# Performance work log

Measured on AMD Instinct MI355X. Metric: run time of the kernel, lower is better.

The kernel has to match this reference:

```python
import jax, jax.numpy as jnp
from jax import lax
import numpy as np
import math

_DN = ('NCHW', 'OIHW', 'NCHW')
_SIGMA = 1.0
_RADIUS = int(4.0 * _SIGMA + 0.5)  # scipy truncate=4.0 default


def _gauss_kernel():
    x = jnp.arange(-_RADIUS, _RADIUS + 1, dtype=jnp.float32)
    k = jnp.exp(-0.5 * x * x / (_SIGMA * _SIGMA))
    return k / k.sum()


def _gaussian_filter(m):
    # m: [B,C,H,W]; scipy mode='reflect' == numpy pad mode 'symmetric'
    B, C, H, W = m.shape
    k = _gauss_kernel()
    x = m.reshape(B * C, 1, H, W)
    xp = jnp.pad(x, ((0, 0), (0, 0), (_RADIUS, _RADIUS), (0, 0)), mode='symmetric')
    x = lax.conv_general_dilated(xp, k.reshape(1, 1, 2 * _RADIUS + 1, 1), (1, 1), 'VALID', dimension_numbers=_DN)
    xp = jnp.pad(x, ((0, 0), (0, 0), (0, 0), (_RADIUS, _RADIUS)), mode='symmetric')
    x = lax.conv_general_dilated(xp, k.reshape(1, 1, 1, 2 * _RADIUS + 1), (1, 1), 'VALID', dimension_numbers=_DN)
    return x.reshape(B, C, H, W)


def _sobel_mag_dir(x):
    C = x.shape[1]
    sx = jnp.array([[-1, 0, 1], [-2, 0, 2], [-1, 0, 1]], dtype=jnp.float32).reshape(1, 1, 3, 3)
    sy = jnp.array([[-1, -2, -1], [0, 0, 0], [1, 2, 1]], dtype=jnp.float32).reshape(1, 1, 3, 3)
    kx = jnp.tile(sx, (C, 1, 1, 1))
    ky = jnp.tile(sy, (C, 1, 1, 1))
    gx = lax.conv_general_dilated(x, kx, (1, 1), ((1, 1), (1, 1)), dimension_numbers=_DN, feature_group_count=C)
    gy = lax.conv_general_dilated(x, ky, (1, 1), ((1, 1), (1, 1)), dimension_numbers=_DN, feature_group_count=C)
    mag = jnp.sqrt(gx * gx + gy * gy + 1e-8)
    direction = jnp.arctan2(gy, gx)
    return mag, direction


def _boundary_weight(mask_f):
    sm = jnp.clip(_gaussian_filter(mask_f), 0.0, 1.0)
    bw = 1.0 - jnp.abs(sm - 0.5) / 0.5
    return jnp.clip(bw, 0.0, 1.0)


def setup_inputs() -> dict:
    key = jax.random.key(0)
    k1, k2, k3 = jax.random.split(key, 3)
    B, C, H, W = 8, 3, 512, 512
    output = jax.random.normal(k1, (B, C, H, W), dtype=jnp.float32)
    target = jax.random.normal(k2, (B, C, H, W), dtype=jnp.float32)
    mask = jax.random.randint(k3, (B, C, H, W), 0, 2, dtype=jnp.int32)
    return {"output": output, "target": target, "mask": mask}


def reference(output, target, mask):
    mask_f = mask.astype(jnp.float32)
    out_mag, out_dir = _sobel_mag_dir(output)
    tgt_mag, tgt_dir = _sobel_mag_dir(target)
    w = _boundary_weight(mask_f)

    mag_loss = jnp.mean(jnp.abs(out_mag * w - tgt_mag * w))
    wsum = w.sum()
    mag_loss = jnp.where(wsum > 0, mag_loss / (w.mean() + 1e-8), mag_loss)

    dd = jnp.abs(out_dir - tgt_dir)
    dd = jnp.minimum(dd, 2 * math.pi - dd)
    dir_loss = (dd * w).sum()
    dir_loss = jnp.where(wsum > 0, dir_loss / (wsum + 1e-8), dir_loss)

    return mag_loss + dir_loss
```

## Files before the change

### kernel.cpp

```cpp
#include <hip/hip_runtime.h>
#include <math.h>

#define HH 512
#define WW 512
#define NBC 24
#define TH 64
#define TW 32
#define RAD 4
#define NXT (WW / TW)
#define NYT (HH / TH)
#define NBLK (NXT * NYT * NBC)
#define PI_F 3.14159265358979323846f
#define SMW 36
#define OTW 40

__device__ __constant__ float GW[9] = {
    1.3383023e-04f, 4.4318484e-03f, 5.3990968e-02f, 2.4197073e-01f,
    3.9894228e-01f, 2.4197073e-01f, 5.3990968e-02f, 4.4318484e-03f,
    1.3383023e-04f
};

__device__ __forceinline__ int reflect_y(int gy)
{
    return (gy < 0) ? (-gy - 1) : ((gy >= HH) ? (2 * HH - 1 - gy) : gy);
}

__device__ __forceinline__ float abs_atan2_fast(float y, float x)
{
    float ax = fabsf(x), ay = fabsf(y);
    float mx = fmaxf(ax, ay), mn = fminf(ax, ay);
    float t = mn * __builtin_amdgcn_rcpf(fmaxf(mx, 1e-30f));
    float s = t * t;
    float r = fmaf(s, fmaf(s, fmaf(s, -0.0851330f, 0.1801410f), -0.3302995f),
                   0.9998660f);
    r = r * t;
    r = (ay > ax) ? (0.5f * PI_F - r) : r;
    r = (x < 0.f) ? (PI_F - r) : r;
    return r;
}

__device__ __forceinline__ float4 hblur12(int4 a, int4 b, int4 c)
{
    float win[12] = {
        (float)a.x, (float)a.y, (float)a.z, (float)a.w,
        (float)b.x, (float)b.y, (float)b.z, (float)b.w,
        (float)c.x, (float)c.y, (float)c.z, (float)c.w };
    float s0 = 0.f, s1 = 0.f, s2 = 0.f, s3 = 0.f;
    #pragma unroll
    for (int j = 0; j < 9; ++j) {
        float gw = GW[j];
        s0 = fmaf(gw, win[j],     s0);
        s1 = fmaf(gw, win[j + 1], s1);
        s2 = fmaf(gw, win[j + 2], s2);
        s3 = fmaf(gw, win[j + 3], s3);
    }
    return make_float4(s0, s1, s2, s3);
}

__device__ __forceinline__ void gload_lds16(const float* gsrc, float* ldst)
{
    __builtin_amdgcn_global_load_lds(
        (const __attribute__((address_space(1))) void*)gsrc,
        (__attribute__((address_space(3))) void*)ldst, 16, 0, 0);
}

__global__ __launch_bounds__(512) void egcl_fused(
    const float* __restrict__ outp,
    const float* __restrict__ tgtp,
    const int*   __restrict__ maskp,
    float*       __restrict__ partials)
{
    __shared__ __align__(16) float smh[TH + 8][SMW];
    __shared__ __align__(16) float oT[TH + 2][OTW];
    __shared__ __align__(16) float tT[TH + 2][OTW];
    __shared__ float red[3][8];

    const int tid  = threadIdx.x;
    const int wv   = tid >> 6;
    const int lane = tid & 63;

    const int bid = (int)blockIdx.x;
    const int nb  = (bid & 7) * (NBLK / 8) + (bid >> 3);
    const int xt  = nb & 15;
    const int yt  = (nb >> 4) & 7;
    const int z   = nb >> 7;
    const int y0  = yt * TH;
    const int x0  = xt * TW;
    const size_t plane = (size_t)z * (HH * WW);
    const bool xedge = (x0 == 0) || (x0 == WW - TW);

    if (!xedge) {
        const int r0  = tid >> 3;
        const int cg0 = (tid & 7) << 2;
        const int gy0 = reflect_y(y0 + r0 - RAD);
        const int* mr0 = maskp + plane + (size_t)gy0 * WW + x0 + cg0;
        int4 ma0 = *(const int4*)(mr0 - 4);
        int4 mb0 = *(const int4*)(mr0);
        int4 mc0 = *(const int4*)(mr0 + 4);
        const bool m2 = (tid < 64);
        int4 ma1 = ma0, mb1 = mb0, mc1 = mc0;
        int r1 = 0;
        if (m2) {
            r1 = 64 + (tid >> 3);
            const int gy1 = reflect_y(y0 + r1 - RAD);
            const int* mr1 = maskp + plane + (size_t)gy1 * WW + x0 + cg0;
            ma1 = *(const int4*)(mr1 - 4);
            mb1 = *(const int4*)(mr1);
            mc1 = *(const int4*)(mr1 + 4);
        }
        asm volatile("" ::: "memory");

        float* oTf = &oT[0][0];
        float* tTf = &tT[0][0];
        for (int seg = wv; seg < 11; seg += 8) {
            int t = (seg << 6) + lane;
            if (t < 660) {
                int rr = t / 10, g = t - 10 * rr;
                int gy = y0 + rr - 1;
                gy = (gy < 0) ? 0 : ((gy >= HH) ? (HH - 1) : gy);
                const size_t off = plane + (size_t)gy * WW + (x0 - 4 + (g << 2));
                gload_lds16(outp + off, oTf + (seg << 8));
                gload_lds16(tgtp + off, tTf + (seg << 8));
            }
        }

        *(float4*)&smh[r0][cg0] = hblur12(ma0, mb0, mc0);
        if (m2) *(float4*)&smh[r1][cg0] = hblur12(ma1, mb1, mc1);

        asm volatile("s_waitcnt vmcnt(0)" ::: "memory");
        if (y0 == 0 && wv == 0 && lane < 10) {
            *(float4*)&oT[0][lane << 2] = make_float4(0.f, 0.f, 0.f, 0.f);
            *(float4*)&tT[0][lane << 2] = make_float4(0.f, 0.f, 0.f, 0.f);
        }
        if (y0 + TH == HH && wv == 2 && lane < 10) {
            *(float4*)&oT[TH + 1][lane << 2] = make_float4(0.f, 0.f, 0.f, 0.f);
            *(float4*)&tT[TH + 1][lane << 2] = make_float4(0.f, 0.f, 0.f, 0.f);
        }
    } else {
        for (int i = tid; i < (TH + 8) * 8; i += 512) {
            int r = i >> 3, cg = (i & 7) << 2;
            int gy = reflect_y(y0 + r - RAD);
            const int* mrow = maskp + plane + (size_t)gy * WW;
            float win[12];
            #pragma unroll
            for (int k = 0; k < 12; ++k) {
                int gx = x0 + cg - 4 + k;
                gx = (gx < 0) ? (-gx - 1) : ((gx >= WW) ? (2 * WW - 1 - gx) : gx);
                win[k] = (float)mrow[gx];
            }
            float s0 = 0.f, s1 = 0.f, s2 = 0.f, s3 = 0.f;
            #pragma unroll
            for (int j = 0; j < 9; ++j) {
                float gw = GW[j];
                s0 = fmaf(gw, win[j],     s0);
                s1 = fmaf(gw, win[j + 1], s1);
                s2 = fmaf(gw, win[j + 2], s2);
                s3 = fmaf(gw, win[j + 3], s3);
            }
            *(float4*)&smh[r][cg] = make_float4(s0, s1, s2, s3);
        }
        for (int i = tid; i < 660; i += 512) {
            int rr = i / 10, g = i - 10 * rr;
            int gy = y0 + rr - 1;
            bool rowin = (gy >= 0) && (gy < HH);
            float a[4], b[4];
            #pragma unroll
            for (int k = 0; k < 4; ++k) {
                int gx = x0 - 4 + 4 * g + k;
                bool in = rowin && (gx >= 0) && (gx < WW);
                size_t idx = plane + (size_t)(rowin ? gy : 0) * WW + (in ? gx : 0);
                a[k] = in ? outp[idx] : 0.f;
                b[k] = in ? tgtp[idx] : 0.f;
            }
            *(float4*)&oT[rr][4 * g] = make_float4(a[0], a[1], a[2], a[3]);
            *(float4*)&tT[rr][4 * g] = make_float4(b[0], b[1], b[2], b[3]);
        }
    }
    __syncthreads();

    const int r  = tid >> 3;
    const int c4 = (tid & 7) << 2;

    float4 a0 = make_float4(0.f, 0.f, 0.f, 0.f);
    #pragma unroll
    for (int j = 0; j < 9; ++j) {
        float4 m = *(const float4*)&smh[r + j][c4];
        float gw = GW[j];
        a0.x = fmaf(gw, m.x, a0.x); a0.y = fmaf(gw, m.y, a0.y);
        a0.z = fmaf(gw, m.z, a0.z); a0.w = fmaf(gw, m.w, a0.w);
    }
    float wgt[4];
    {
        float smv[4] = {a0.x, a0.y, a0.z, a0.w};
        #pragma unroll
        for (int i = 0; i < 4; ++i) {
            float sm = fminf(fmaxf(smv[i], 0.f), 1.f);
            wgt[i] = fmaf(-2.f, fabsf(sm - 0.5f), 1.f);
        }
    }

    float Wo[3][8], Wt[3][8];
    #pragma unroll
    for (int j = 0; j < 3; ++j) {
        *(float2*)&Wo[j][0] = *(const float2*)&oT[r + j][c4 + 2];
        *(float4*)&Wo[j][2] = *(const float4*)&oT[r + j][c4 + 4];
        *(float2*)&Wo[j][6] = *(const float2*)&oT[r + j][c4 + 8];
        *(float2*)&Wt[j][0] = *(const float2*)&tT[r + j][c4 + 2];
        *(float4*)&Wt[j][2] = *(const float4*)&tT[r + j][c4 + 4];
        *(float2*)&Wt[j][6] = *(const float2*)&tT[r + j][c4 + 8];
    }

    float to_[6], uo[6], tt_[6], ut[6];
    #pragma unroll
    for (int j = 0; j < 6; ++j) {
        to_[j] = fmaf(2.f, Wo[1][j + 1], Wo[0][j + 1] + Wo[2][j + 1]);
        uo[j]  = Wo[2][j + 1] - Wo[0][j + 1];
        tt_[j] = fmaf(2.f, Wt[1][j + 1], Wt[0][j + 1] + Wt[2][j + 1]);
        ut[j]  = Wt[2][j + 1] - Wt[0][j + 1];
    }

    float s_w = 0.f, s_mag = 0.f, s_dir = 0.f;
    #pragma unroll
    for (int i = 0; i < 4; ++i) {
        float xo = to_[i + 2] - to_[i];
        float yo = fmaf(2.f, uo[i + 1], uo[i] + uo[i + 2]);
        float xt_ = tt_[i + 2] - tt_[i];
        float yt_ = fmaf(2.f, ut[i + 1], ut[i] + ut[i + 2]);

        float mago = __builtin_amdgcn_sqrtf(fmaf(xo, xo, fmaf(yo, yo, 1e-8f)));
        float magt = __builtin_amdgcn_sqrtf(fmaf(xt_, xt_, fmaf(yt_, yt_, 1e-8f)));
        float cross = yo * xt_ - xo * yt_;
        float dotp  = fmaf(xo, xt_, yo * yt_);
        float dd = abs_atan2_fast(cross, dotp);
        float w = wgt[i];
        s_w   += w;
        s_mag += w * fabsf(mago - magt);
        s_dir += dd * w;
    }

    #pragma unroll
    for (int o = 32; o > 0; o >>= 1) {
        s_w   += __shfl_down(s_w,   o, 64);
        s_mag += __shfl_down(s_mag, o, 64);
        s_dir += __shfl_down(s_dir, o, 64);
    }
    const int wid = tid >> 6;
    if ((tid & 63) == 0) { red[0][wid] = s_w; red[1][wid] = s_mag; red[2][wid] = s_dir; }
    __syncthreads();
    if (tid == 0) {
        float p0 = 0.f, p1 = 0.f, p2 = 0.f;
        #pragma unroll
        for (int k = 0; k < 8; ++k) { p0 += red[0][k]; p1 += red[1][k]; p2 += red[2][k]; }
        partials[bid]            = p0;
        partials[NBLK + bid]     = p1;
        partials[2 * NBLK + bid] = p2;
    }
}

__global__ __launch_bounds__(256) void egcl_finalize(
    const float* __restrict__ partials, float* __restrict__ out)
{
    __shared__ double red[3][4];
    const int tid = threadIdx.x;
    double s0 = 0.0, s1 = 0.0, s2 = 0.0;
    const float4* p0 = (const float4*)partials;
    const float4* p1 = (const float4*)(partials + NBLK);
    const float4* p2 = (const float4*)(partials + 2 * NBLK);
    for (int i = tid; i < NBLK / 4; i += 256) {
        float4 a = p0[i], b = p1[i], c = p2[i];
        s0 += (double)a.x + (double)a.y + (double)a.z + (double)a.w;
        s1 += (double)b.x + (double)b.y + (double)b.z + (double)b.w;
        s2 += (double)c.x + (double)c.y + (double)c.z + (double)c.w;
    }
    #pragma unroll
    for (int o = 32; o > 0; o >>= 1) {
        s0 += __shfl_down(s0, o, 64);
        s1 += __shfl_down(s1, o, 64);
        s2 += __shfl_down(s2, o, 64);
    }
    const int wid = tid >> 6;
    if ((tid & 63) == 0) { red[0][wid] = s0; red[1][wid] = s1; red[2][wid] = s2; }
    __syncthreads();
    if (tid == 0) {
        double Sw   = red[0][0] + red[0][1] + red[0][2] + red[0][3];
        double Smag = red[1][0] + red[1][1] + red[1][2] + red[1][3];
        double Sdir = red[2][0] + red[2][1] + red[2][2] + red[2][3];
        const double N = (double)NBC * HH * WW;
        double mag_loss = Smag / N;
        if (Sw > 0.0) mag_loss = mag_loss / (Sw / N + 1e-8);
        double dir_loss = Sdir;
        if (Sw > 0.0) dir_loss = Sdir / (Sw + 1e-8);
        out[0] = (float)(mag_loss + dir_loss);
    }
}

extern "C" void kernel_launch(void* const* d_in, const int* in_sizes, int n_in,
                              void* d_out, int out_size, void* d_ws, size_t ws_size,
                              hipStream_t stream)
{
    const float* outp = (const float*)d_in[0];
    const float* tgtp = (const float*)d_in[1];
    const int*   maskp = (const int*)d_in[2];
    float* partials = (float*)d_ws;

    egcl_fused<<<dim3(NBLK, 1, 1), 512, 0, stream>>>(outp, tgtp, maskp, partials);
    egcl_finalize<<<1, 256, 0, stream>>>(partials, (float*)d_out);
}
```

Measured before the change: 34.80 us.

## Process two adjacent tiles per block with double-buffered LDS staging

Each block now handles two horizontally adjacent 32-wide tiles instead of one, so the grid is halved. The second tile's async global-to-LDS loads and mask blur are issued before the first tile is computed, which overlaps memory latency with compute. The cost is doubled LDS per block, which may reduce occupancy, and fewer blocks to spread across CUs. The per-block partials and the finalize kernel are resized to match.

```diff
diff --git a/kernel.cpp b/kernel.cpp
--- a/kernel.cpp
+++ b/kernel.cpp
@@ -7,9 +7,7 @@
 #define TH 64
 #define TW 32
 #define RAD 4
-#define NXT (WW / TW)
-#define NYT (HH / TH)
-#define NBLK (NXT * NYT * NBC)
+#define NPAIR 1536
 #define PI_F 3.14159265358979323846f
 #define SMW 36
 #define OTW 40
@@ -70,9 +68,9 @@
     const int*   __restrict__ maskp,
     float*       __restrict__ partials)
 {
-    __shared__ __align__(16) float smh[TH + 8][SMW];
-    __shared__ __align__(16) float oT[TH + 2][OTW];
-    __shared__ __align__(16) float tT[TH + 2][OTW];
+    __shared__ __align__(16) float smh[2][TH + 8][SMW];
+    __shared__ __align__(16) float oT[2][TH + 2][OTW];
+    __shared__ __align__(16) float tT[2][TH + 2][OTW];
     __shared__ float red[3][8];
 
     const int tid  = threadIdx.x;
@@ -80,38 +78,20 @@
     const int lane = tid & 63;
 
     const int bid = (int)blockIdx.x;
-    const int nb  = (bid & 7) * (NBLK / 8) + (bid >> 3);
-    const int xt  = nb & 15;
-    const int yt  = (nb >> 4) & 7;
-    const int z   = nb >> 7;
+    const int nb  = (bid & 7) * (NPAIR / 8) + (bid >> 3);
+    const int px  = nb & 7;
+    const int yt  = (nb >> 3) & 7;
+    const int z   = nb >> 6;
     const int y0  = yt * TH;
-    const int x0  = xt * TW;
+    const int x0A = px * 64;
+    const int x0B = x0A + TW;
     const size_t plane = (size_t)z * (HH * WW);
-    const bool xedge = (x0 == 0) || (x0 == WW - TW);
-
-    if (!xedge) {
-        const int r0  = tid >> 3;
-        const int cg0 = (tid & 7) << 2;
-        const int gy0 = reflect_y(y0 + r0 - RAD);
-        const int* mr0 = maskp + plane + (size_t)gy0 * WW + x0 + cg0;
-        int4 ma0 = *(const int4*)(mr0 - 4);
-        int4 mb0 = *(const int4*)(mr0);
-        int4 mc0 = *(const int4*)(mr0 + 4);
-        const bool m2 = (tid < 64);
-        int4 ma1 = ma0, mb1 = mb0, mc1 = mc0;
-        int r1 = 0;
-        if (m2) {
-            r1 = 64 + (tid >> 3);
-            const int gy1 = reflect_y(y0 + r1 - RAD);
-            const int* mr1 = maskp + plane + (size_t)gy1 * WW + x0 + cg0;
-            ma1 = *(const int4*)(mr1 - 4);
-            mb1 = *(const int4*)(mr1);
-            mc1 = *(const int4*)(mr1 + 4);
-        }
-        asm volatile("" ::: "memory");
-
-        float* oTf = &oT[0][0];
-        float* tTf = &tT[0][0];
+    const bool edgeA = (px == 0);
+    const bool edgeB = (px == 7);
+
+    auto dma_ot = [&](int b, int x0) {
+        float* oTf = &oT[b][0][0];
+        float* tTf = &tT[b][0][0];
         for (int seg = wv; seg < 11; seg += 8) {
             int t = (seg << 6) + lane;
             if (t < 660) {
@@ -123,120 +103,161 @@
                 gload_lds16(tgtp + off, tTf + (seg << 8));
             }
         }
-
-        *(float4*)&smh[r0][cg0] = hblur12(ma0, mb0, mc0);
-        if (m2) *(float4*)&smh[r1][cg0] = hblur12(ma1, mb1, mc1);
-
-        asm volatile("s_waitcnt vmcnt(0)" ::: "memory");
+    };
+    auto fixup = [&](int b) {
         if (y0 == 0 && wv == 0 && lane < 10) {
-            *(float4*)&oT[0][lane << 2] = make_float4(0.f, 0.f, 0.f, 0.f);
-            *(float4*)&tT[0][lane << 2] = make_float4(0.f, 0.f, 0.f, 0.f);
+            *(float4*)&oT[b][0][lane << 2] = make_float4(0.f, 0.f, 0.f, 0.f);
+            *(float4*)&tT[b][0][lane << 2] = make_float4(0.f, 0.f, 0.f, 0.f);
         }
         if (y0 + TH == HH && wv == 2 && lane < 10) {
-            *(float4*)&oT[TH + 1][lane << 2] = make_float4(0.f, 0.f, 0.f, 0.f);
-            *(float4*)&tT[TH + 1][lane << 2] = make_float4(0.f, 0.f, 0.f, 0.f);
-        }
-    } else {
-        for (int i = tid; i < (TH + 8) * 8; i += 512) {
-            int r = i >> 3, cg = (i & 7) << 2;
-            int gy = reflect_y(y0 + r - RAD);
-            const int* mrow = maskp + plane + (size_t)gy * WW;
-            float win[12];
-            #pragma unroll
-            for (int k = 0; k < 12; ++k) {
-                int gx = x0 + cg - 4 + k;
-                gx = (gx < 0) ? (-gx - 1) : ((gx >= WW) ? (2 * WW - 1 - gx) : gx);
-                win[k] = (float)mrow[gx];
-            }
-            float s0 = 0.f, s1 = 0.f, s2 = 0.f, s3 = 0.f;
-            #pragma unroll
-            for (int j = 0; j < 9; ++j) {
-                float gw = GW[j];
-                s0 = fmaf(gw, win[j],     s0);
-                s1 = fmaf(gw, win[j + 1], s1);
-                s2 = fmaf(gw, win[j + 2], s2);
-                s3 = fmaf(gw, win[j + 3], s3);
-            }
-            *(float4*)&smh[r][cg] = make_float4(s0, s1, s2, s3);
-        }
+            *(float4*)&oT[b][TH + 1][lane << 2] = make_float4(0.f, 0.f, 0.f, 0.f);
+            *(float4*)&tT[b][TH + 1][lane << 2] = make_float4(0.f, 0.f, 0.f, 0.f);
+        }
+    };
+    auto stage_mask = [&](int b, int x0, bool xedge) {
+        if (!xedge) {
+            const int r0  = tid >> 3;
+            const int cg0 = (tid & 7) << 2;
+            const int gy0 = reflect_y(y0 + r0 - RAD);
+            const int* mr0 = maskp + plane + (size_t)gy0 * WW + x0 + cg0;
+            int4 ma0 = *(const int4*)(mr0 - 4);
+            int4 mb0 = *(const int4*)(mr0);
+            int4 mc0 = *(const int4*)(mr0 + 4);
+            *(float4*)&smh[b][r0][cg0] = hblur12(ma0, mb0, mc0);
+            if (tid < 64) {
+                const int r1 = 64 + (tid >> 3);
+                const int gy1 = reflect_y(y0 + r1 - RAD);
+                const int* mr1 = maskp + plane + (size_t)gy1 * WW + x0 + cg0;
+                int4 ma1 = *(const int4*)(mr1 - 4);
+                int4 mb1 = *(const int4*)(mr1);
+                int4 mc1 = *(const int4*)(mr1 + 4);
+                *(float4*)&smh[b][r1][cg0] = hblur12(ma1, mb1, mc1);
+            }
+        } else {
+            for (int i = tid; i < (TH + 8) * 8; i += 512) {
+                int r = i >> 3, cg = (i & 7) << 2;
+                int gy = reflect_y(y0 + r - RAD);
+                const int* mrow = maskp + plane + (size_t)gy * WW;
+                float win[12];
+                #pragma unroll
+                for (int k = 0; k < 12; ++k) {
+                    int gx = x0 + cg - 4 + k;
+                    gx = (gx < 0) ? (-gx - 1) : ((gx >= WW) ? (2 * WW - 1 - gx) : gx);
+                    win[k] = (float)mrow[gx];
+                }
+                float s0 = 0.f, s1 = 0.f, s2 = 0.f, s3 = 0.f;
+                #pragma unroll
+                for (int j = 0; j < 9; ++j) {
+                    float gw = GW[j];
+                    s0 = fmaf(gw, win[j],     s0);
+                    s1 = fmaf(gw, win[j + 1], s1);
+                    s2 = fmaf(gw, win[j + 2], s2);
+                    s3 = fmaf(gw, win[j + 3], s3);
+                }
+                *(float4*)&smh[b][r][cg] = make_float4(s0, s1, s2, s3);
+            }
+        }
+    };
+    auto stage_ot_scalar = [&](int b, int x0) {
         for (int i = tid; i < 660; i += 512) {
             int rr = i / 10, g = i - 10 * rr;
             int gy = y0 + rr - 1;
             bool rowin = (gy >= 0) && (gy < HH);
-            float a[4], b[4];
+            float a[4], c[4];
             #pragma unroll
             for (int k = 0; k < 4; ++k) {
                 int gx = x0 - 4 + 4 * g + k;
                 bool in = rowin && (gx >= 0) && (gx < WW);
                 size_t idx = plane + (size_t)(rowin ? gy : 0) * WW + (in ? gx : 0);
                 a[k] = in ? outp[idx] : 0.f;
-                b[k] = in ? tgtp[idx] : 0.f;
-            }
-            *(float4*)&oT[rr][4 * g] = make_float4(a[0], a[1], a[2], a[3]);
-            *(float4*)&tT[rr][4 * g] = make_float4(b[0], b[1], b[2], b[3]);
-        }
+                c[k] = in ? tgtp[idx] : 0.f;
+            }
+            *(float4*)&oT[b][rr][4 * g] = make_float4(a[0], a[1], a[2], a[3]);
+            *(float4*)&tT[b][rr][4 * g] = make_float4(c[0], c[1], c[2], c[3]);
+        }
+    };
+
+    float s_w = 0.f, s_mag = 0.f, s_dir = 0.f;
+
+    auto compute = [&](int b) {
+        const int r  = tid >> 3;
+        const int c4 = (tid & 7) << 2;
+        float4 a0 = make_float4(0.f, 0.f, 0.f, 0.f);
+        #pragma unroll
+        for (int j = 0; j < 9; ++j) {
+            float4 m = *(const float4*)&smh[b][r + j][c4];
+            float gw = GW[j];
+            a0.x = fmaf(gw, m.x, a0.x); a0.y = fmaf(gw, m.y, a0.y);
+            a0.z = fmaf(gw, m.z, a0.z); a0.w = fmaf(gw, m.w, a0.w);
+        }
+        float wgt[4];
+        {
+            float smv[4] = {a0.x, a0.y, a0.z, a0.w};
+            #pragma unroll
+            for (int i = 0; i < 4; ++i) {
+                float sm = fminf(fmaxf(smv[i], 0.f), 1.f);
+                wgt[i] = fmaf(-2.f, fabsf(sm - 0.5f), 1.f);
+            }
+        }
+        float Wo[3][8], Wt[3][8];
+        #pragma unroll
+        for (int j = 0; j < 3; ++j) {
+            *(float2*)&Wo[j][0] = *(const float2*)&oT[b][r + j][c4 + 2];
+            *(float4*)&Wo[j][2] = *(const float4*)&oT[b][r + j][c4 + 4];
+            *(float2*)&Wo[j][6] = *(const float2*)&oT[b][r + j][c4 + 8];
+            *(float2*)&Wt[j][0] = *(const float2*)&tT[b][r + j][c4 + 2];
+            *(float4*)&Wt[j][2] = *(const float4*)&tT[b][r + j][c4 + 4];
+            *(float2*)&Wt[j][6] = *(const float2*)&tT[b][r + j][c4 + 8];
+        }
+        float to_[6], uo[6], tt_[6], ut[6];
+        #pragma unroll
+        for (int j = 0; j < 6; ++j) {
+            to_[j] = fmaf(2.f, Wo[1][j + 1], Wo[0][j + 1] + Wo[2][j + 1]);
+            uo[j]  = Wo[2][j + 1] - Wo[0][j + 1];
+            tt_[j] = fmaf(2.f, Wt[1][j + 1], Wt[0][j + 1] + Wt[2][j + 1]);
+            ut[j]  = Wt[2][j + 1] - Wt[0][j + 1];
+        }
+        #pragma unroll
+        for (int i = 0; i < 4; ++i) {
+            float xo = to_[i + 2] - to_[i];
+            float yo = fmaf(2.f, uo[i + 1], uo[i] + uo[i + 2]);
+            float xt_ = tt_[i + 2] - tt_[i];
+            float yt_ = fmaf(2.f, ut[i + 1], ut[i] + ut[i + 2]);
+            float mago = __builtin_amdgcn_sqrtf(fmaf(xo, xo, fmaf(yo, yo, 1e-8f)));
+            float magt = __builtin_amdgcn_sqrtf(fmaf(xt_, xt_, fmaf(yt_, yt_, 1e-8f)));
+            float cross = yo * xt_ - xo * yt_;
+            float dotp  = fmaf(xo, xt_, yo * yt_);
+            float dd = abs_atan2_fast(cross, dotp);
+            float w = wgt[i];
+            s_w   += w;
+            s_mag += w * fabsf(mago - magt);
+            s_dir += dd * w;
+        }
+    };
+
+    if (!edgeA) {
+        dma_ot(0, x0A);
+        stage_mask(0, x0A, false);
+        asm volatile("s_waitcnt vmcnt(0)" ::: "memory");
+        fixup(0);
+    } else {
+        stage_mask(0, x0A, true);
+        stage_ot_scalar(0, x0A);
     }
     __syncthreads();
 
-    const int r  = tid >> 3;
-    const int c4 = (tid & 7) << 2;
-
-    float4 a0 = make_float4(0.f, 0.f, 0.f, 0.f);
-    #pragma unroll
-    for (int j = 0; j < 9; ++j) {
-        float4 m = *(const float4*)&smh[r + j][c4];
-        float gw = GW[j];
-        a0.x = fmaf(gw, m.x, a0.x); a0.y = fmaf(gw, m.y, a0.y);
-        a0.z = fmaf(gw, m.z, a0.z); a0.w = fmaf(gw, m.w, a0.w);
-    }
-    float wgt[4];
-    {
-        float smv[4] = {a0.x, a0.y, a0.z, a0.w};
-        #pragma unroll
-        for (int i = 0; i < 4; ++i) {
-            float sm = fminf(fmaxf(smv[i], 0.f), 1.f);
-            wgt[i] = fmaf(-2.f, fabsf(sm - 0.5f), 1.f);
-        }
-    }
-
-    float Wo[3][8], Wt[3][8];
-    #pragma unroll
-    for (int j = 0; j < 3; ++j) {
-        *(float2*)&Wo[j][0] = *(const float2*)&oT[r + j][c4 + 2];
-        *(float4*)&Wo[j][2] = *(const float4*)&oT[r + j][c4 + 4];
-        *(float2*)&Wo[j][6] = *(const float2*)&oT[r + j][c4 + 8];
-        *(float2*)&Wt[j][0] = *(const float2*)&tT[r + j][c4 + 2];
-        *(float4*)&Wt[j][2] = *(const float4*)&tT[r + j][c4 + 4];
-        *(float2*)&Wt[j][6] = *(const float2*)&tT[r + j][c4 + 8];
-    }
-
-    float to_[6], uo[6], tt_[6], ut[6];
-    #pragma unroll
-    for (int j = 0; j < 6; ++j) {
-        to_[j] = fmaf(2.f, Wo[1][j + 1], Wo[0][j + 1] + Wo[2][j + 1]);
-        uo[j]  = Wo[2][j + 1] - Wo[0][j + 1];
-        tt_[j] = fmaf(2.f, Wt[1][j + 1], Wt[0][j + 1] + Wt[2][j + 1]);
-        ut[j]  = Wt[2][j + 1] - Wt[0][j + 1];
-    }
-
-    float s_w = 0.f, s_mag = 0.f, s_dir = 0.f;
-    #pragma unroll
-    for (int i = 0; i < 4; ++i) {
-        float xo = to_[i + 2] - to_[i];
-        float yo = fmaf(2.f, uo[i + 1], uo[i] + uo[i + 2]);
-        float xt_ = tt_[i + 2] - tt_[i];
-        float yt_ = fmaf(2.f, ut[i + 1], ut[i] + ut[i + 2]);
-
-        float mago = __builtin_amdgcn_sqrtf(fmaf(xo, xo, fmaf(yo, yo, 1e-8f)));
-        float magt = __builtin_amdgcn_sqrtf(fmaf(xt_, xt_, fmaf(yt_, yt_, 1e-8f)));
-        float cross = yo * xt_ - xo * yt_;
-        float dotp  = fmaf(xo, xt_, yo * yt_);
-        float dd = abs_atan2_fast(cross, dotp);
-        float w = wgt[i];
-        s_w   += w;
-        s_mag += w * fabsf(mago - magt);
-        s_dir += dd * w;
-    }
+    if (!edgeB) dma_ot(1, x0B);
+    stage_mask(1, x0B, edgeB);
+    compute(0);
+    if (!edgeB) {
+        asm volatile("s_waitcnt vmcnt(0)" ::: "memory");
+        fixup(1);
+    } else {
+        stage_ot_scalar(1, x0B);
+    }
+    __syncthreads();
+
+    compute(1);
 
     #pragma unroll
     for (int o = 32; o > 0; o >>= 1) {
@@ -251,9 +272,9 @@
         float p0 = 0.f, p1 = 0.f, p2 = 0.f;
         #pragma unroll
         for (int k = 0; k < 8; ++k) { p0 += red[0][k]; p1 += red[1][k]; p2 += red[2][k]; }
-        partials[bid]            = p0;
-        partials[NBLK + bid]     = p1;
-        partials[2 * NBLK + bid] = p2;
+        partials[bid]             = p0;
+        partials[NPAIR + bid]     = p1;
+        partials[2 * NPAIR + bid] = p2;
     }
 }
 
@@ -264,9 +285,9 @@
     const int tid = threadIdx.x;
     double s0 = 0.0, s1 = 0.0, s2 = 0.0;
     const float4* p0 = (const float4*)partials;
-    const float4* p1 = (const float4*)(partials + NBLK);
-    const float4* p2 = (const float4*)(partials + 2 * NBLK);
-    for (int i = tid; i < NBLK / 4; i += 256) {
+    const float4* p1 = (const float4*)(partials + NPAIR);
+    const float4* p2 = (const float4*)(partials + 2 * NPAIR);
+    for (int i = tid; i < NPAIR / 4; i += 256) {
         float4 a = p0[i], b = p1[i], c = p2[i];
         s0 += (double)a.x + (double)a.y + (double)a.z + (double)a.w;
         s1 += (double)b.x + (double)b.y + (double)b.z + (double)b.w;
@@ -303,6 +324,6 @@
     const int*   maskp = (const int*)d_in[2];
     float* partials = (float*)d_ws;
 
-    egcl_fused<<<dim3(NBLK, 1, 1), 512, 0, stream>>>(outp, tgtp, maskp, partials);
+    egcl_fused<<<dim3(NPAIR, 1, 1), 512, 0, stream>>>(outp, tgtp, maskp, partials);
     egcl_finalize<<<1, 256, 0, stream>>>(partials, (float*)d_out);
 }
```

New measurement: 39.18 us. 12.6% more time.
